# Kernel optimization log

Measured on AMD Instinct MI355X. Metric: run time of the kernel, lower is better.

The kernel has to match this reference:

```python
import jax, jax.numpy as jnp
import numpy as np

B, L, KDIM, QDIM, ADIM, ODIM, H = 4, 1024, 1024, 1024, 1024, 1024, 16
DK = ADIM // H
SCALE = float(np.sqrt(DK))
NEG_INF = float(np.finfo(np.float32).min)


def setup_inputs() -> dict:
    key = jax.random.key(0)
    ks = jax.random.split(key, 12)
    s = 0.02
    return {
        "key": jax.random.normal(ks[0], (B, L, KDIM), jnp.float32),
        "value": jax.random.normal(ks[1], (B, L, KDIM), jnp.float32),
        "query": jax.random.normal(ks[2], (B, L, QDIM), jnp.float32),
        "mask": jax.random.randint(ks[3], (B, L, L), 0, 2, jnp.int32),
        "Wk": jax.random.normal(ks[4], (ADIM, KDIM), jnp.float32) * s,
        "bk": jnp.zeros((ADIM,), jnp.float32),
        "Wv": jax.random.normal(ks[5], (ADIM, KDIM), jnp.float32) * s,
        "bv": jnp.zeros((ADIM,), jnp.float32),
        "Wq": jax.random.normal(ks[6], (ADIM, QDIM), jnp.float32) * s,
        "bq": jnp.zeros((ADIM,), jnp.float32),
        "Wo": jax.random.normal(ks[7], (ODIM, ADIM), jnp.float32) * s,
        "bo": jnp.zeros((ODIM,), jnp.float32),
    }


def reference(key, value, query, mask, Wk, bk, Wv, bv, Wq, bq, Wo, bo):
    bs, klen = key.shape[0], key.shape[1]
    qlen = query.shape[1]
    # projections -> [B, len, H, d_k]
    k = (key @ Wk.T + bk).reshape(bs, klen, H, DK)
    v = (value @ Wv.T + bv).reshape(bs, klen, H, DK)
    q = (query @ Wq.T + bq).reshape(bs, qlen, H, DK)
    # attention energy [B, qlen, klen, H]
    e = jnp.einsum('bihd,bjhd->bijh', q, k) / SCALE
    m = mask[:, :, :, None]  # [B,q,k,1] broadcasts over heads
    e = jnp.where(m == 0, NEG_INF, e)
    aw = jax.nn.softmax(e, axis=2)  # softmax over klen
    cv = jnp.einsum('bijh,bjhd->bihd', aw, v).reshape(bs, qlen, ADIM)
    cv = cv @ Wo.T + bo
    return cv, jnp.transpose(aw, (0, 3, 1, 2))  # [B,H,q,k]
```

## Files before the change

### kernel.cpp

```cpp
#include <hip/hip_runtime.h>
#include <hip/hip_bf16.h>

typedef __attribute__((ext_vector_type(8))) __bf16 bf16x8;
typedef __attribute__((ext_vector_type(8))) short short8;
typedef __attribute__((ext_vector_type(4))) short s16x4;
typedef __attribute__((ext_vector_type(4))) float f32x4;

#define LN 1024
#define NH 16
#define DKH 64

__device__ __forceinline__ short f2bf(float f) {
    unsigned u = __builtin_bit_cast(unsigned, f);
    u = u + 0x7fffu + ((u >> 16) & 1u);
    return (short)(u >> 16);
}
__device__ __forceinline__ float bf2f(short s) {
    return __builtin_bit_cast(float, ((unsigned)(unsigned short)s) << 16);
}

__device__ __forceinline__ void gl_lds16(const short* g, short* l) {
    __builtin_amdgcn_global_load_lds(
        (const __attribute__((address_space(1))) void*)g,
        (__attribute__((address_space(3))) void*)l, 16, 0, 0);
}

__global__ __launch_bounds__(256) void prep_all(
    const float* __restrict__ q, const float* __restrict__ k, const float* __restrict__ v,
    const float* __restrict__ wq, const float* __restrict__ wk,
    const float* __restrict__ wv, const float* __restrict__ wo,
    short* __restrict__ dq, short* __restrict__ dk, short* __restrict__ dv,
    short* __restrict__ dwq, short* __restrict__ dwk,
    short* __restrict__ dwv, short* __restrict__ dwo,
    const int* __restrict__ mask, unsigned long long* __restrict__ bits)
{
    int bid = blockIdx.x;
    if (bid < 8192) {
        const float* s; short* d; int base;
        if      (bid < 2048) { s = q;  d = dq;  base = bid; }
        else if (bid < 4096) { s = k;  d = dk;  base = bid - 2048; }
        else if (bid < 6144) { s = v;  d = dv;  base = bid - 4096; }
        else if (bid < 6656) { s = wq; d = dwq; base = bid - 6144; }
        else if (bid < 7168) { s = wk; d = dwk; base = bid - 6656; }
        else if (bid < 7680) { s = wv; d = dwv; base = bid - 7168; }
        else                 { s = wo; d = dwo; base = bid - 7680; }
        int i = base * 256 + threadIdx.x;
        f32x4 a = ((const f32x4*)s)[i * 2];
        f32x4 b = ((const f32x4*)s)[i * 2 + 1];
        short8 o;
        #pragma unroll
        for (int j = 0; j < 4; ++j) { o[j] = f2bf(a[j]); o[4 + j] = f2bf(b[j]); }
        ((short8*)d)[i] = o;
    } else {
        int mid = bid - 8192;
        const int i = mid & 1023;
        const int b = mid >> 10;
        const int qq = threadIdx.x >> 6;
        const int lane = threadIdx.x & 63;
        const int* mp = &mask[((size_t)b * LN + i) * LN + qq * 256 + lane * 4];
        int4 mv = *(const int4*)mp;
        unsigned long long b0 = __ballot(mv.x != 0);
        unsigned long long b1 = __ballot(mv.y != 0);
        unsigned long long b2 = __ballot(mv.z != 0);
        unsigned long long b3 = __ballot(mv.w != 0);
        if (lane == 0) {
            unsigned long long* o = &bits[(((size_t)b * LN + i) * 4 + qq) * 4];
            o[0] = b0; o[1] = b1; o[2] = b2; o[3] = b3;
        }
    }
}

template<int MODE>
__device__ __forceinline__ void gemm_body(
    const short* __restrict__ A, const short* __restrict__ Bt,
    const float* __restrict__ bias, void* __restrict__ Cp,
    int m0, int n0, int N, int K, short* lA, short* lB)
{
    const int tid = threadIdx.x;
    const int lane = tid & 63;
    const int wid = tid >> 6;
    const int wr = wid >> 1, wc = wid & 1;
    const int lr = lane & 15, lg = lane >> 4;

    int srow[2], skc[2];
    #pragma unroll
    for (int p = 0; p < 2; ++p) {
        int ch = p * 256 + wid * 64 + lane;
        srow[p] = ch >> 3;
        skc[p] = (((ch & 7) ^ (srow[p] & 7))) * 8;
    }

    f32x4 acc[2][2] = {};

    for (int k0 = 0; k0 < K; k0 += 64) {
        #pragma unroll
        for (int p = 0; p < 2; ++p) {
            gl_lds16(A  + (size_t)(m0 + srow[p]) * K + k0 + skc[p], &lA[(p * 256 + wid * 64) * 8]);
            gl_lds16(Bt + (size_t)(n0 + srow[p]) * K + k0 + skc[p], &lB[(p * 256 + wid * 64) * 8]);
        }
        __syncthreads();
        bf16x8 af[2][2], bfr[2][2];
        #pragma unroll
        for (int kh = 0; kh < 2; ++kh) {
            #pragma unroll
            for (int m = 0; m < 2; ++m) {
                int arow = wr * 32 + m * 16 + lr;
                af[kh][m] = *(const bf16x8*)&lA[arow * 64 + (((kh * 4 + lg) ^ (arow & 7)) * 8)];
            }
            #pragma unroll
            for (int n = 0; n < 2; ++n) {
                int brow = wc * 32 + n * 16 + lr;
                bfr[kh][n] = *(const bf16x8*)&lB[brow * 64 + (((kh * 4 + lg) ^ (brow & 7)) * 8)];
            }
        }
        #pragma unroll
        for (int kh = 0; kh < 2; ++kh)
            #pragma unroll
            for (int m = 0; m < 2; ++m)
                #pragma unroll
                for (int n = 0; n < 2; ++n)
                    acc[m][n] = __builtin_amdgcn_mfma_f32_16x16x32_bf16(af[kh][m], bfr[kh][n], acc[m][n], 0, 0, 0);
        __syncthreads();
    }

    #pragma unroll
    for (int m = 0; m < 2; ++m)
        #pragma unroll
        for (int n = 0; n < 2; ++n) {
            int col = n0 + wc * 32 + n * 16 + lr;
            float bb = bias[col];
            if (MODE == 1) {
                int row = m0 + wr * 32 + m * 16 + lg * 4;
                int bb_i = row >> 10, tok = row & 1023;
                int hh = col >> 6, dd = col & 63;
                s16x4 o;
                #pragma unroll
                for (int r = 0; r < 4; ++r) o[r] = f2bf(acc[m][n][r] + bb);
                *(s16x4*)&((short*)Cp)[((size_t)((bb_i * NH + hh) * DKH) + dd) * LN + tok] = o;
            } else {
                #pragma unroll
                for (int r = 0; r < 4; ++r) {
                    int row = m0 + wr * 32 + m * 16 + lg * 4 + r;
                    float v = acc[m][n][r] + bb;
                    if (MODE == 2) ((float*)Cp)[(size_t)row * N + col] = v;
                    else           ((short*)Cp)[(size_t)row * N + col] = f2bf(v);
                }
            }
        }
}

template<int MODE>
__device__ __forceinline__ void gemm_body128(
    const short* __restrict__ A, const short* __restrict__ Bt,
    const float* __restrict__ bias, void* __restrict__ Cp,
    int m0, int n0, int N, int K, short* lA, short* lB)
{
    const int tid = threadIdx.x;
    const int lane = tid & 63;
    const int wid = tid >> 6;
    const int wr = wid >> 1, wc = wid & 1;
    const int lr = lane & 15, lg = lane >> 4;

    int srow[4], skc[4];
    #pragma unroll
    for (int p = 0; p < 4; ++p) {
        int ch = p * 256 + wid * 64 + lane;
        srow[p] = ch >> 3;
        skc[p] = (((ch & 7) ^ (srow[p] & 7))) * 8;
    }

    f32x4 acc[4][4] = {};

    for (int k0 = 0; k0 < K; k0 += 64) {
        #pragma unroll
        for (int p = 0; p < 4; ++p) {
            gl_lds16(A  + (size_t)(m0 + srow[p]) * K + k0 + skc[p], &lA[(p * 256 + wid * 64) * 8]);
            gl_lds16(Bt + (size_t)(n0 + srow[p]) * K + k0 + skc[p], &lB[(p * 256 + wid * 64) * 8]);
        }
        __syncthreads();
        #pragma unroll
        for (int kh = 0; kh < 2; ++kh) {
            bf16x8 af[4], bfr[4];
            #pragma unroll
            for (int m = 0; m < 4; ++m) {
                int arow = wr * 64 + m * 16 + lr;
                af[m] = *(const bf16x8*)&lA[arow * 64 + (((kh * 4 + lg) ^ (arow & 7)) * 8)];
            }
            #pragma unroll
            for (int n = 0; n < 4; ++n) {
                int brow = wc * 64 + n * 16 + lr;
                bfr[n] = *(const bf16x8*)&lB[brow * 64 + (((kh * 4 + lg) ^ (brow & 7)) * 8)];
            }
            #pragma unroll
            for (int m = 0; m < 4; ++m)
                #pragma unroll
                for (int n = 0; n < 4; ++n)
                    acc[m][n] = __builtin_amdgcn_mfma_f32_16x16x32_bf16(af[m], bfr[n], acc[m][n], 0, 0, 0);
        }
        __syncthreads();
    }

    #pragma unroll
    for (int m = 0; m < 4; ++m)
        #pragma unroll
        for (int n = 0; n < 4; ++n) {
            int col = n0 + wc * 64 + n * 16 + lr;
            float bb = bias[col];
            if (MODE == 1) {
                int row = m0 + wr * 64 + m * 16 + lg * 4;
                int bb_i = row >> 10, tok = row & 1023;
                int hh = col >> 6, dd = col & 63;
                s16x4 o;
                #pragma unroll
                for (int r = 0; r < 4; ++r) o[r] = f2bf(acc[m][n][r] + bb);
                *(s16x4*)&((short*)Cp)[((size_t)((bb_i * NH + hh) * DKH) + dd) * LN + tok] = o;
            } else {
                #pragma unroll
                for (int r = 0; r < 4; ++r) {
                    int row = m0 + wr * 64 + m * 16 + lg * 4 + r;
                    float v = acc[m][n][r] + bb;
                    if (MODE == 2) ((float*)Cp)[(size_t)row * N + col] = v;
                    else           ((short*)Cp)[(size_t)row * N + col] = f2bf(v);
                }
            }
        }
}

__global__ __launch_bounds__(256) void gemm_qkv128(
    const short* __restrict__ vin, const short* __restrict__ qin, const short* __restrict__ kin,
    const short* __restrict__ wv, const short* __restrict__ wq, const short* __restrict__ wk,
    const float* __restrict__ bv, const float* __restrict__ bq, const float* __restrict__ bk,
    short* __restrict__ vT, short* __restrict__ q_bf, short* __restrict__ k_bf)
{
    __shared__ short lA[128 * 64];
    __shared__ short lB[128 * 64];
    const int m0 = blockIdx.y * 128, n0 = blockIdx.x * 128;
    if (blockIdx.z == 0)
        gemm_body128<1>(vin, wv, bv, vT, m0, n0, 1024, 1024, lA, lB);
    else if (blockIdx.z == 1)
        gemm_body128<0>(qin, wq, bq, q_bf, m0, n0, 1024, 1024, lA, lB);
    else
        gemm_body128<0>(kin, wk, bk, k_bf, m0, n0, 1024, 1024, lA, lB);
}

__global__ __launch_bounds__(256) void gemm_vq(
    const short* __restrict__ vin, const short* __restrict__ qin,
    const short* __restrict__ wv, const short* __restrict__ wq,
    const float* __restrict__ bv, const float* __restrict__ bq,
    short* __restrict__ vT, short* __restrict__ q_bf)
{
    __shared__ short lA[64 * 64];
    __shared__ short lB[64 * 64];
    const int m0 = blockIdx.y * 64, n0 = blockIdx.x * 64;
    if (blockIdx.z == 0)
        gemm_body<1>(vin, wv, bv, vT, m0, n0, 1024, 1024, lA, lB);
    else
        gemm_body<0>(qin, wq, bq, q_bf, m0, n0, 1024, 1024, lA, lB);
}

__global__ __launch_bounds__(256) void gemm_bf(
    const short* __restrict__ A, const short* __restrict__ Bt,
    const float* __restrict__ bias, short* __restrict__ C)
{
    __shared__ short lA[64 * 64];
    __shared__ short lB[64 * 64];
    gemm_body<0>(A, Bt, bias, C, blockIdx.y * 64, blockIdx.x * 64, 1024, 1024, lA, lB);
}

__global__ __launch_bounds__(256) void gemm_out(
    const short* __restrict__ A, const short* __restrict__ Bt,
    const float* __restrict__ bias, float* __restrict__ C)
{
    __shared__ short lA[64 * 64];
    __shared__ short lB[64 * 64];
    gemm_body<2>(A, Bt, bias, C, blockIdx.y * 64, blockIdx.x * 64, 1024, 1024, lA, lB);
}

__global__ __launch_bounds__(256, 2) void attn_kernel(
    const short* __restrict__ qb, const short* __restrict__ kb,
    const short* __restrict__ vT, const unsigned long long* __restrict__ mb,
    float* __restrict__ aw, short* __restrict__ cv)
{
    __shared__ short p_lds[32 * 1024];
    __shared__ float redbuf[4][32];

    const int bid = blockIdx.x;
    const int swz = (bid & 7) * 256 + (bid >> 3);
    const int i0 = (swz & 31) * 32;
    const int h = (swz >> 5) & 15;
    const int b = swz >> 9;

    const int tid = threadIdx.x;
    const int lane = tid & 63;
    const int w = tid >> 6;
    const int lr = lane & 15, lg = lane >> 4;

    unsigned long long Bm[2][4];
    #pragma unroll
    for (int g = 0; g < 2; ++g)
        #pragma unroll
        for (int r = 0; r < 4; ++r)
            Bm[g][r] = mb[(((size_t)b * LN + i0 + g * 16 + lg * 4 + r) * 4 + w) * 4 + (lr & 3)] >> (lr >> 2);

    bf16x8 a0[2], a1[2];
    #pragma unroll
    for (int g = 0; g < 2; ++g) {
        const short* qp = &qb[((size_t)b * LN + i0 + g * 16 + lr) * 1024 + h * 64 + lg * 8];
        a0[g] = *(const bf16x8*)qp;
        a1[g] = *(const bf16x8*)(qp + 32);
    }

    f32x4 acc[2][16];
    #pragma unroll
    for (int g = 0; g < 2; ++g)
        #pragma unroll
        for (int jf = 0; jf < 16; ++jf) acc[g][jf] = f32x4{0.f, 0.f, 0.f, 0.f};

    const size_t krow_base = (size_t)b * LN;
    #pragma unroll
    for (int jf = 0; jf < 16; ++jf) {
        int j0f = w * 256 + jf * 16;
        const short* kp = &kb[(krow_base + j0f + lr) * 1024 + h * 64 + lg * 8];
        bf16x8 b0 = *(const bf16x8*)kp;
        bf16x8 b1 = *(const bf16x8*)(kp + 32);
        acc[0][jf] = __builtin_amdgcn_mfma_f32_16x16x32_bf16(a0[0], b0, acc[0][jf], 0, 0, 0);
        acc[0][jf] = __builtin_amdgcn_mfma_f32_16x16x32_bf16(a1[0], b1, acc[0][jf], 0, 0, 0);
        acc[1][jf] = __builtin_amdgcn_mfma_f32_16x16x32_bf16(a0[1], b0, acc[1][jf], 0, 0, 0);
        acc[1][jf] = __builtin_amdgcn_mfma_f32_16x16x32_bf16(a1[1], b1, acc[1][jf], 0, 0, 0);
    }

    float ps[2][4] = {};
    #pragma unroll
    for (int g = 0; g < 2; ++g)
        #pragma unroll
        for (int jf = 0; jf < 16; ++jf)
            #pragma unroll
            for (int r = 0; r < 4; ++r) {
                float p = ((Bm[g][r] >> (jf * 4)) & 1ULL) ? __expf(acc[g][jf][r] * 0.125f) : 0.0f;
                acc[g][jf][r] = p;
                ps[g][r] += p;
            }

    #pragma unroll
    for (int g = 0; g < 2; ++g)
        #pragma unroll
        for (int r = 0; r < 4; ++r) {
            for (int off = 1; off < 16; off <<= 1) ps[g][r] += __shfl_xor(ps[g][r], off, 64);
        }
    if (lr == 0) {
        #pragma unroll
        for (int g = 0; g < 2; ++g)
            #pragma unroll
            for (int r = 0; r < 4; ++r) redbuf[w][g * 16 + lg * 4 + r] = ps[g][r];
    }

    #pragma unroll
    for (int g = 0; g < 2; ++g)
        #pragma unroll
        for (int jf = 0; jf < 16; ++jf) {
            int j = w * 256 + jf * 16 + lr;
            #pragma unroll
            for (int r = 0; r < 4; ++r) {
                int row = g * 16 + lg * 4 + r;
                int byte = (row * 2048 + j * 2) ^ ((row & 7) << 4);
                *(short*)((char*)p_lds + byte) = f2bf(acc[g][jf][r]);
            }
        }
    __syncthreads();

    f32x4 accA[2] = {}, accB[2] = {};
    const int d0 = w * 16;
    const short* vrow = vT + ((size_t)((b * NH + h) * DKH) + d0 + lr) * LN;
    #pragma unroll
    for (int ks = 0; ks < 32; ks += 2) {
        bf16x8 vb0 = *(const bf16x8*)&vrow[ks * 32 + lg * 8];
        bf16x8 vb1 = *(const bf16x8*)&vrow[(ks + 1) * 32 + lg * 8];
        #pragma unroll
        for (int g = 0; g < 2; ++g) {
            int row = g * 16 + lr;
            int byte0 = (row * 2048 + (ks * 32 + lg * 8) * 2) ^ ((row & 7) << 4);
            int byte1 = (row * 2048 + ((ks + 1) * 32 + lg * 8) * 2) ^ ((row & 7) << 4);
            bf16x8 pa0 = *(const bf16x8*)((char*)p_lds + byte0);
            bf16x8 pa1 = *(const bf16x8*)((char*)p_lds + byte1);
            accA[g] = __builtin_amdgcn_mfma_f32_16x16x32_bf16(pa0, vb0, accA[g], 0, 0, 0);
            accB[g] = __builtin_amdgcn_mfma_f32_16x16x32_bf16(pa1, vb1, accB[g], 0, 0, 0);
        }
    }

    float inv[2][4];
    #pragma unroll
    for (int g = 0; g < 2; ++g)
        #pragma unroll
        for (int r = 0; r < 4; ++r) {
            float s = redbuf[0][g * 16 + lg * 4 + r];
            for (int ww = 1; ww < 4; ++ww) s += redbuf[ww][g * 16 + lg * 4 + r];
            inv[g][r] = 1.0f / s;
        }
    #pragma unroll
    for (int g = 0; g < 2; ++g)
        #pragma unroll
        for (int r = 0; r < 4; ++r) {
            int irow = i0 + g * 16 + lg * 4 + r;
            cv[((size_t)b * LN + irow) * 1024 + h * 64 + d0 + lr] = f2bf((accA[g][r] + accB[g][r]) * inv[g][r]);
        }

    {
        const int arow = tid >> 3;
        const int ac0 = tid & 7;
        float s = redbuf[0][arow] + redbuf[1][arow] + redbuf[2][arow] + redbuf[3][arow];
        float ainv = 1.0f / s;
        float* awr = aw + ((size_t)(b * NH + h) * LN + i0 + arow) * LN;
        const int abase = arow * 2048;
        const int aswz = (arow & 7) << 4;
        #pragma unroll
        for (int it = 0; it < 16; ++it) {
            int k = ac0 + it * 8;
            int byte = (abase + k * 16) ^ aswz;
            short8 pv = *(const short8*)((char*)p_lds + byte);
            f32x4 o0, o1;
            #pragma unroll
            for (int j = 0; j < 4; ++j) {
                o0[j] = bf2f(pv[j]) * ainv;
                o1[j] = bf2f(pv[4 + j]) * ainv;
            }
            *(f32x4*)&awr[k * 8] = o0;
            *(f32x4*)&awr[k * 8 + 4] = o1;
        }
    }
}

extern "C" void kernel_launch(void* const* d_in, const int* in_sizes, int n_in,
                              void* d_out, int out_size, void* d_ws, size_t ws_size,
                              hipStream_t stream) {
    (void)in_sizes; (void)n_in; (void)out_size;
    const float* key   = (const float*)d_in[0];
    const float* value = (const float*)d_in[1];
    const float* query = (const float*)d_in[2];
    const int*   mask  = (const int*)d_in[3];
    const float* Wk = (const float*)d_in[4];
    const float* bk = (const float*)d_in[5];
    const float* Wv = (const float*)d_in[6];
    const float* bv = (const float*)d_in[7];
    const float* Wq = (const float*)d_in[8];
    const float* bq = (const float*)d_in[9];
    const float* Wo = (const float*)d_in[10];
    const float* bo = (const float*)d_in[11];

    float* out_cv = (float*)d_out;
    float* out_aw = out_cv + (size_t)4096 * 1024;

    unsigned long long* mbits_g = (unsigned long long*)out_cv;
    short* q_bf = (short*)((char*)d_out + (size_t)(1u << 19));

    const size_t MB = 1u << 20;
    char* ws = (char*)d_ws;
    short* qin  = (short*)(ws + 0 * MB);
    short* kin  = (short*)(ws + 8 * MB);   short* cv_bf = kin;
    short* vin  = (short*)(ws + 16 * MB);
    short* wq   = (short*)(ws + 24 * MB);
    short* wk   = (short*)(ws + 26 * MB);
    short* wv   = (short*)(ws + 28 * MB);
    short* wo   = (short*)(ws + 30 * MB);
    short* vT   = (short*)(ws + 32 * MB);

    dim3 blk(256);
    prep_all<<<dim3(12288), blk, 0, stream>>>(
        query, key, value, Wq, Wk, Wv, Wo,
        qin, kin, vin, wq, wk, wv, wo,
        mask, mbits_g);

    if (ws_size >= (size_t)48 * MB) {
        short* k_bf = (short*)(ws + 40 * MB);
        gemm_qkv128<<<dim3(8, 32, 3), blk, 0, stream>>>(
            vin, qin, kin, wv, wq, wk, bv, bq, bk, vT, q_bf, k_bf);
        attn_kernel<<<dim3(2048), blk, 0, stream>>>(q_bf, k_bf, vT, mbits_g, out_aw, cv_bf);
    } else {
        short* k_bf = qin;
        gemm_vq<<<dim3(16, 64, 2), blk, 0, stream>>>(vin, qin, wv, wq, bv, bq, vT, q_bf);
        gemm_bf<<<dim3(16, 64), blk, 0, stream>>>(kin, wk, bk, k_bf);
        attn_kernel<<<dim3(2048), blk, 0, stream>>>(q_bf, k_bf, vT, mbits_g, out_aw, cv_bf);
    }
    gemm_out<<<dim3(16, 64), blk, 0, stream>>>(cv_bf, wo, bo, out_cv);
}
```

Before: 198.6 us.

## Split attention block work across 8 waves instead of 4

The attention kernel now runs 512 threads per block. Each wave covers 128 key columns instead of 256 in QK^T/softmax, and the PV stage is split so each wave handles one 16-row group and one 16-wide d slice. The mask bit extraction, reduction buffer and aw writeback loop are adjusted to match. This halves per-thread accumulator registers and adds in-flight waves per CU to hide memory latency. The cost is more cross-wave reduction work and some duplicated V loads across the row groups.

```diff
diff --git a/kernel.cpp b/kernel.cpp
--- a/kernel.cpp
+++ b/kernel.cpp
@@ -276,13 +276,13 @@
     gemm_body<2>(A, Bt, bias, C, blockIdx.y * 64, blockIdx.x * 64, 1024, 1024, lA, lB);
 }
 
-__global__ __launch_bounds__(256, 2) void attn_kernel(
+__global__ __launch_bounds__(512, 4) void attn_kernel(
     const short* __restrict__ qb, const short* __restrict__ kb,
     const short* __restrict__ vT, const unsigned long long* __restrict__ mb,
     float* __restrict__ aw, short* __restrict__ cv)
 {
     __shared__ short p_lds[32 * 1024];
-    __shared__ float redbuf[4][32];
+    __shared__ float redbuf[8][32];
 
     const int bid = blockIdx.x;
     const int swz = (bid & 7) * 256 + (bid >> 3);
@@ -300,7 +300,8 @@
     for (int g = 0; g < 2; ++g)
         #pragma unroll
         for (int r = 0; r < 4; ++r)
-            Bm[g][r] = mb[(((size_t)b * LN + i0 + g * 16 + lg * 4 + r) * 4 + w) * 4 + (lr & 3)] >> (lr >> 2);
+            Bm[g][r] = mb[(((size_t)b * LN + i0 + g * 16 + lg * 4 + r) * 4 + (w >> 1)) * 4 + (lr & 3)]
+                       >> ((w & 1) * 32 + (lr >> 2));
 
     bf16x8 a0[2], a1[2];
     #pragma unroll
@@ -310,16 +311,16 @@
         a1[g] = *(const bf16x8*)(qp + 32);
     }
 
-    f32x4 acc[2][16];
+    f32x4 acc[2][8];
     #pragma unroll
     for (int g = 0; g < 2; ++g)
         #pragma unroll
-        for (int jf = 0; jf < 16; ++jf) acc[g][jf] = f32x4{0.f, 0.f, 0.f, 0.f};
+        for (int jf = 0; jf < 8; ++jf) acc[g][jf] = f32x4{0.f, 0.f, 0.f, 0.f};
 
     const size_t krow_base = (size_t)b * LN;
     #pragma unroll
-    for (int jf = 0; jf < 16; ++jf) {
-        int j0f = w * 256 + jf * 16;
+    for (int jf = 0; jf < 8; ++jf) {
+        int j0f = w * 128 + jf * 16;
         const short* kp = &kb[(krow_base + j0f + lr) * 1024 + h * 64 + lg * 8];
         bf16x8 b0 = *(const bf16x8*)kp;
         bf16x8 b1 = *(const bf16x8*)(kp + 32);
@@ -333,7 +334,7 @@
     #pragma unroll
     for (int g = 0; g < 2; ++g)
         #pragma unroll
-        for (int jf = 0; jf < 16; ++jf)
+        for (int jf = 0; jf < 8; ++jf)
             #pragma unroll
             for (int r = 0; r < 4; ++r) {
                 float p = ((Bm[g][r] >> (jf * 4)) & 1ULL) ? __expf(acc[g][jf][r] * 0.125f) : 0.0f;
@@ -357,8 +358,8 @@
     #pragma unroll
     for (int g = 0; g < 2; ++g)
         #pragma unroll
-        for (int jf = 0; jf < 16; ++jf) {
-            int j = w * 256 + jf * 16 + lr;
+        for (int jf = 0; jf < 8; ++jf) {
+            int j = w * 128 + jf * 16 + lr;
             #pragma unroll
             for (int r = 0; r < 4; ++r) {
                 int row = g * 16 + lg * 4 + r;
@@ -368,53 +369,52 @@
         }
     __syncthreads();
 
-    f32x4 accA[2] = {}, accB[2] = {};
-    const int d0 = w * 16;
+    const int gp = w >> 2;
+    const int d0 = (w & 3) * 16;
+    f32x4 accA = {0.f, 0.f, 0.f, 0.f}, accB = {0.f, 0.f, 0.f, 0.f};
     const short* vrow = vT + ((size_t)((b * NH + h) * DKH) + d0 + lr) * LN;
+    const int prow = gp * 16 + lr;
+    const int pbase = prow * 2048;
+    const int pswz = (prow & 7) << 4;
     #pragma unroll
     for (int ks = 0; ks < 32; ks += 2) {
         bf16x8 vb0 = *(const bf16x8*)&vrow[ks * 32 + lg * 8];
         bf16x8 vb1 = *(const bf16x8*)&vrow[(ks + 1) * 32 + lg * 8];
-        #pragma unroll
-        for (int g = 0; g < 2; ++g) {
-            int row = g * 16 + lr;
-            int byte0 = (row * 2048 + (ks * 32 + lg * 8) * 2) ^ ((row & 7) << 4);
-            int byte1 = (row * 2048 + ((ks + 1) * 32 + lg * 8) * 2) ^ ((row & 7) << 4);
-            bf16x8 pa0 = *(const bf16x8*)((char*)p_lds + byte0);
-            bf16x8 pa1 = *(const bf16x8*)((char*)p_lds + byte1);
-            accA[g] = __builtin_amdgcn_mfma_f32_16x16x32_bf16(pa0, vb0, accA[g], 0, 0, 0);
-            accB[g] = __builtin_amdgcn_mfma_f32_16x16x32_bf16(pa1, vb1, accB[g], 0, 0, 0);
-        }
-    }
-
-    float inv[2][4];
-    #pragma unroll
-    for (int g = 0; g < 2; ++g)
-        #pragma unroll
-        for (int r = 0; r < 4; ++r) {
-            float s = redbuf[0][g * 16 + lg * 4 + r];
-            for (int ww = 1; ww < 4; ++ww) s += redbuf[ww][g * 16 + lg * 4 + r];
-            inv[g][r] = 1.0f / s;
-        }
-    #pragma unroll
-    for (int g = 0; g < 2; ++g)
-        #pragma unroll
-        for (int r = 0; r < 4; ++r) {
-            int irow = i0 + g * 16 + lg * 4 + r;
-            cv[((size_t)b * LN + irow) * 1024 + h * 64 + d0 + lr] = f2bf((accA[g][r] + accB[g][r]) * inv[g][r]);
-        }
+        int byte0 = (pbase + (ks * 32 + lg * 8) * 2) ^ pswz;
+        int byte1 = (pbase + ((ks + 1) * 32 + lg * 8) * 2) ^ pswz;
+        bf16x8 pa0 = *(const bf16x8*)((char*)p_lds + byte0);
+        bf16x8 pa1 = *(const bf16x8*)((char*)p_lds + byte1);
+        accA = __builtin_amdgcn_mfma_f32_16x16x32_bf16(pa0, vb0, accA, 0, 0, 0);
+        accB = __builtin_amdgcn_mfma_f32_16x16x32_bf16(pa1, vb1, accB, 0, 0, 0);
+    }
+
+    float invp[4];
+    #pragma unroll
+    for (int r = 0; r < 4; ++r) {
+        float s = redbuf[0][gp * 16 + lg * 4 + r];
+        #pragma unroll
+        for (int ww = 1; ww < 8; ++ww) s += redbuf[ww][gp * 16 + lg * 4 + r];
+        invp[r] = 1.0f / s;
+    }
+    #pragma unroll
+    for (int r = 0; r < 4; ++r) {
+        int irow = i0 + gp * 16 + lg * 4 + r;
+        cv[((size_t)b * LN + irow) * 1024 + h * 64 + d0 + lr] = f2bf((accA[r] + accB[r]) * invp[r]);
+    }
 
     {
-        const int arow = tid >> 3;
-        const int ac0 = tid & 7;
-        float s = redbuf[0][arow] + redbuf[1][arow] + redbuf[2][arow] + redbuf[3][arow];
+        const int arow = tid >> 4;
+        const int ac0 = tid & 15;
+        float s = 0.f;
+        #pragma unroll
+        for (int ww = 0; ww < 8; ++ww) s += redbuf[ww][arow];
         float ainv = 1.0f / s;
         float* awr = aw + ((size_t)(b * NH + h) * LN + i0 + arow) * LN;
         const int abase = arow * 2048;
         const int aswz = (arow & 7) << 4;
         #pragma unroll
-        for (int it = 0; it < 16; ++it) {
-            int k = ac0 + it * 8;
+        for (int it = 0; it < 8; ++it) {
+            int k = ac0 + it * 16;
             int byte = (abase + k * 16) ^ aswz;
             short8 pv = *(const short8*)((char*)p_lds + byte);
             f32x4 o0, o1;
@@ -473,12 +473,12 @@
         short* k_bf = (short*)(ws + 40 * MB);
         gemm_qkv128<<<dim3(8, 32, 3), blk, 0, stream>>>(
             vin, qin, kin, wv, wq, wk, bv, bq, bk, vT, q_bf, k_bf);
-        attn_kernel<<<dim3(2048), blk, 0, stream>>>(q_bf, k_bf, vT, mbits_g, out_aw, cv_bf);
+        attn_kernel<<<dim3(2048), dim3(512), 0, stream>>>(q_bf, k_bf, vT, mbits_g, out_aw, cv_bf);
     } else {
         short* k_bf = qin;
         gemm_vq<<<dim3(16, 64, 2), blk, 0, stream>>>(vin, qin, wv, wq, bv, bq, vT, q_bf);
         gemm_bf<<<dim3(16, 64), blk, 0, stream>>>(kin, wk, bk, k_bf);
-        attn_kernel<<<dim3(2048), blk, 0, stream>>>(q_bf, k_bf, vT, mbits_g, out_aw, cv_bf);
+        attn_kernel<<<dim3(2048), dim3(512), 0, stream>>>(q_bf, k_bf, vT, mbits_g, out_aw, cv_bf);
     }
     gemm_out<<<dim3(16, 64), blk, 0, stream>>>(cv_bf, wo, bo, out_cv);
 }
```

Result: slower. 220.7 us (+11.2%).
